# Kernel optimization log

Measured on AMD Instinct MI355X. Metric: run time of the kernel, lower is better.

Reference implementation:

```python
import jax, jax.numpy as jnp
import numpy as np

B, T, N = 16, 1024, 128
WIN, STEP = 30, 2
MOMENT_ORDERS = (2, 4, 8)
D_MODEL = 256


def _mask_diag(corr):
    n = corr.shape[-1]
    eye = jnp.eye(n, dtype=corr.dtype)
    return corr * (1.0 - eye) + eye


def corrcoef_time(xw):
    # xw: [..., L, N] -> corr over channels: [..., N, N]
    L = xw.shape[-2]
    xm = xw - xw.mean(axis=-2, keepdims=True)
    cov = jnp.einsum('...ln,...lm->...nm', xm, xm) / (L - 1 + 1e-8)
    var = jnp.clip(jnp.diagonal(cov, axis1=-2, axis2=-1), 1e-8, None)
    std = jnp.sqrt(var)
    corr = cov / (std[..., :, None] * std[..., None, :])
    corr = jnp.nan_to_num(corr, nan=0.0, posinf=0.0, neginf=0.0)
    return _mask_diag(corr)


def rowwise_corr(M):
    # M: [B, N, F]
    Xc = M - M.mean(axis=-1, keepdims=True)
    num = jnp.einsum('bnf,bmf->bnm', Xc, Xc)
    den1 = jnp.sqrt(jnp.clip((Xc ** 2).sum(axis=-1), 1e-8, None))
    corr = num / (den1[:, :, None] * den1[:, None, :])
    corr = jnp.nan_to_num(corr, nan=0.0, posinf=0.0, neginf=0.0)
    return _mask_diag(corr)


def layer_norm(x, gamma, beta, eps=1e-5):
    mu = x.mean(axis=-1, keepdims=True)
    var = ((x - mu) ** 2).mean(axis=-1, keepdims=True)
    return (x - mu) / jnp.sqrt(var + eps) * gamma + beta


def normalize_adj(adj):
    n = adj.shape[-1]
    A_hat = adj + jnp.eye(n, dtype=adj.dtype)
    d = A_hat.sum(axis=-1)
    dis = jnp.sqrt(1.0 / jnp.clip(d, 1e-8, None))
    return A_hat * dis[:, :, None] * dis[:, None, :]


def setup_inputs() -> dict:
    key = jax.random.key(0)
    ks = jax.random.split(key, 8)
    in_dim = len(MOMENT_ORDERS) * N
    return {
        'x': jax.random.normal(ks[0], (B, T, N), dtype=jnp.float32),
        'ln_gamma': jnp.ones((in_dim,), jnp.float32),
        'ln_beta': jnp.zeros((in_dim,), jnp.float32),
        'W1': jax.random.normal(ks[1], (in_dim, D_MODEL), jnp.float32) * 0.05,
        'b1': jnp.zeros((D_MODEL,), jnp.float32),
        'W2': jax.random.normal(ks[2], (D_MODEL, D_MODEL), jnp.float32) * 0.05,
        'b2': jnp.zeros((D_MODEL,), jnp.float32),
        'Wc': jax.random.normal(ks[3], (D_MODEL, 1), jnp.float32) * 0.05,
        'bc': jnp.zeros((1,), jnp.float32),
    }


def reference(x, ln_gamma, ln_beta, W1, b1, W2, b2, Wc, bc):
    # sliding windows (static indices)
    starts = np.arange(0, T - WIN + 1, STEP)
    idx = starts[:, None] + np.arange(WIN)[None, :]
    xw = x[:, idx, :]
    lo = corrcoef_time(xw)                            # [B, Wn, N, N]

    mean_lo = lo.mean(axis=1, keepdims=True)
    centered = lo - mean_lo
    cm_list, ho_list = [], []
    for d in MOMENT_ORDERS:
        cm = jnp.nan_to_num((centered ** d).mean(axis=1),
                            nan=0.0, posinf=0.0, neginf=0.0)  # [B, N, N]
        cm_list.append(cm)
        ho_list.append(rowwise_corr(cm))

    X = jnp.concatenate(cm_list, axis=-1)             # [B, N, 3N]
    X = layer_norm(X, ln_gamma, ln_beta)

    A = jnp.stack(ho_list, axis=1).mean(axis=1)
    A = 0.5 * (A + jnp.swapaxes(A, 1, 2))
    A_norm = normalize_adj(A)

    H = jax.nn.relu(jnp.einsum('bnm,bmd->bnd', A_norm, X @ W1 + b1))
    H = jax.nn.relu(jnp.einsum('bnm,bmd->bnd', A_norm, H @ W2 + b2))
    g = H.mean(axis=1)                                # [B, d_model]
    out = jax.nn.sigmoid(g @ Wc + bc)                 # [B, 1]
    return out
```

## Files before the change

kernel.cpp:

```cpp
#include <hip/hip_runtime.h>
#include <math.h>

#define BB  16
#define TT  1024
#define NN  128
#define WIN 30
#define NWD 498
#define DM  256
#define IND 384
#define GW  9

#define INV_W (1.0f/498.0f)

#define SARR (BB*NN*NN)

#define OFF_A     0
#define OFF_G     (OFF_A    + BB*NWD*NN)
#define OFF_CM2   (OFF_G    + BB*NWD*NN)
#define OFF_CM4   (OFF_CM2  + SARR)
#define OFF_CM8   (OFF_CM4  + SARR)
#define OFF_PART  (OFF_CM8  + SARR)
#define OFF_ASUM  OFF_PART
#define OFF_ANORM (OFF_ASUM + SARR)
#define OFF_X     (OFF_ANORM + SARR)
#define OFF_BUFA  (OFF_X    + BB*NN*IND)
#define OFF_BUFB  (OFF_BUFA + BB*NN*DM)

__global__ __launch_bounds__(128) void k1_stats(const float* __restrict__ x, float* __restrict__ ws) {
    int bx = blockIdx.x;
    int c = bx & 15, b = bx >> 4;
    int w0 = c*32, w1 = min(NWD, w0+32);
    int n = threadIdx.x;
    const float* xp = x + (size_t)b*TT*NN + n;

    float sum = 0.f, sq = 0.f;
    for (int t = 2*w0; t < 2*w0 + WIN; ++t) {
        float v = xp[(size_t)t*NN];
        sum += v; sq = fmaf(v, v, sq);
    }
    for (int w = w0; w < w1; ++w) {
        if (w > w0) {
            float o0 = xp[(size_t)(2*w-2)*NN], o1 = xp[(size_t)(2*w-1)*NN];
            float n0 = xp[(size_t)(2*w+28)*NN], n1 = xp[(size_t)(2*w+29)*NN];
            sum += (n0 + n1) - (o0 + o1);
            sq  += (n0*n0 + n1*n1) - (o0*o0 + o1*o1);
        }
        float mean = sum * (1.0f/30.0f);
        float ss = sq - 30.0f*mean*mean;
        float var = fmaxf(ss * (1.0f/29.0f), 1e-8f);
        float a = (1.0f / sqrtf(var)) * 0.185695338f;
        ws[OFF_A + ((size_t)b*NWD + w)*NN + n] = a;
        ws[OFF_G + ((size_t)b*NWD + w)*NN + n] = mean * a * 5.477225575f;
    }
}

__global__ __launch_bounds__(256) __attribute__((amdgpu_waves_per_eu(3, 3)))
void k24_inc(const float* __restrict__ x, float* __restrict__ ws) {
    __shared__ __align__(16) float xr[64][NN];
    __shared__ __align__(16) float sa[GW][NN];
    __shared__ __align__(16) float sg[GW][NN];
    int bx = blockIdx.x;
    int wc = bx & 7;
    int slab = (bx >> 3) % 6;
    int b = bx / 48;
    const char IS[6] = {0,0,0,0,1,1};
    const char JS[6] = {0,1,2,3,2,3};
    int is = IS[slab], js = JS[slab];
    int w0 = wc * 63, w1 = min(NWD, w0 + 63);
    int tid = threadIdx.x;
    int jg = tid & 7, ig = tid >> 3;
    int i0 = is*64 + ig*2;
    int j0 = js*32 + jg*4;

    const float* xb = x + (size_t)b*TT*NN;
    const float* Ab = ws + OFF_A + (size_t)b*NWD*NN;
    const float* Gb = ws + OFF_G + (size_t)b*NWD*NN;

    float P[2][4];
    float S1[2][4], S2[2][4], S3[2][4], S4[2][4], S5[2][4], S6[2][4], S7[2][4], S8[2][4];
#pragma unroll
    for (int p=0;p<2;++p)
#pragma unroll
        for (int q=0;q<4;++q) {
            P[p][q]=0.f;
            S1[p][q]=0.f;S2[p][q]=0.f;S3[p][q]=0.f;S4[p][q]=0.f;
            S5[p][q]=0.f;S6[p][q]=0.f;S7[p][q]=0.f;S8[p][q]=0.f;
        }

    auto moments = [&](int k) {
        float2 ai = *(const float2*)&sa[k][i0];
        float2 gi = *(const float2*)&sg[k][i0];
        float4 aj = *(const float4*)&sa[k][j0];
        float4 gj = *(const float4*)&sg[k][j0];
        float av[2] = {ai.x, ai.y};
        float mg[2] = {-gi.x, -gi.y};
        float aw[4] = {aj.x, aj.y, aj.z, aj.w};
        float gw[4] = {gj.x, gj.y, gj.z, gj.w};
#pragma unroll
        for (int p=0;p<2;++p)
#pragma unroll
            for (int q=0;q<4;++q) {
                float aa  = av[p]*aw[q];
                float ngg = mg[p]*gw[q];
                float c   = fmaf(P[p][q], aa, ngg);
                float c2 = c*c;
                float c3 = c2*c;
                float c4 = c2*c2;
                S1[p][q] += c;
                S2[p][q] += c2;
                S3[p][q] += c3;
                S4[p][q] += c4;
                S5[p][q] = fmaf(c4, c,  S5[p][q]);
                S6[p][q] = fmaf(c3, c3, S6[p][q]);
                S7[p][q] = fmaf(c3, c4, S7[p][q]);
                S8[p][q] = fmaf(c4, c4, S8[p][q]);
            }
    };

    int rlo = 2*w0;
    for (int wg = w0; wg < w1; wg += GW) {
        int m = min(GW, w1 - wg);
        __syncthreads();
        int rhi = 2*(wg + m - 1) + 29;
        int nr = rhi - rlo + 1;
        for (int idx = tid; idx < nr*32; idx += 256) {
            int r = idx >> 5, c4 = idx & 31;
            int t = rlo + r;
            *(float4*)&xr[t & 63][c4*4] = ((const float4*)(xb + (size_t)t*NN))[c4];
        }
        for (int idx = tid; idx < m*32; idx += 256) {
            int k = idx >> 5, c4 = idx & 31;
            *(float4*)&sa[k][c4*4] = ((const float4*)(Ab + (size_t)(wg+k)*NN))[c4];
        }
        for (int idx = tid; idx < m*32; idx += 256) {
            int k = idx >> 5, c4 = idx & 31;
            *(float4*)&sg[k][c4*4] = ((const float4*)(Gb + (size_t)(wg+k)*NN))[c4];
        }
        rlo = rhi + 1;
        __syncthreads();

        int kstart = 0;
        if (wg == w0) {
#pragma unroll 6
            for (int k = 0; k < WIN; ++k) {
                int t = 2*w0 + k;
                float2 xi = *(const float2*)&xr[t & 63][i0];
                float4 xj = *(const float4*)&xr[t & 63][j0];
                float av[2] = {xi.x, xi.y};
                float bv[4] = {xj.x, xj.y, xj.z, xj.w};
#pragma unroll
                for (int p=0;p<2;++p)
#pragma unroll
                    for (int q=0;q<4;++q) P[p][q] = fmaf(av[p], bv[q], P[p][q]);
            }
            moments(0);
            kstart = 1;
        }
        for (int k = kstart; k < m; ++k) {
            int w = wg + k;
            int tr[4] = {2*w - 2, 2*w - 1, 2*w + 28, 2*w + 29};
#pragma unroll
            for (int kk = 0; kk < 4; ++kk) {
                int t = tr[kk];
                float sgn = (kk < 2) ? -1.0f : 1.0f;
                float2 xi = *(const float2*)&xr[t & 63][i0];
                float4 xj = *(const float4*)&xr[t & 63][j0];
                float av[2] = {sgn*xi.x, sgn*xi.y};
                float bv[4] = {xj.x, xj.y, xj.z, xj.w};
#pragma unroll
                for (int p=0;p<2;++p)
#pragma unroll
                    for (int q=0;q<4;++q) P[p][q] = fmaf(av[p], bv[q], P[p][q]);
            }
            moments(k);
        }
    }

    float* tp = ws + OFF_PART + (size_t)bx*16384 + tid*8;
#define STORE_ARR(A, S) \
    *(float4*)&tp[(A)*2048]     = make_float4(S[0][0], S[0][1], S[0][2], S[0][3]); \
    *(float4*)&tp[(A)*2048 + 4] = make_float4(S[1][0], S[1][1], S[1][2], S[1][3]);
    STORE_ARR(0, S1) STORE_ARR(1, S2) STORE_ARR(2, S3) STORE_ARR(3, S4)
    STORE_ARR(4, S5) STORE_ARR(5, S6) STORE_ARR(6, S7) STORE_ARR(7, S8)
#undef STORE_ARR
}

__global__ __launch_bounds__(256) void kred(float* __restrict__ ws) {
    int pair = blockIdx.x;
    int b = pair / 6, slab = pair % 6;
    const char IS[6] = {0,0,0,0,1,1};
    const char JS[6] = {0,1,2,3,2,3};
    int is = IS[slab], js = JS[slab];
    int tid = threadIdx.x;
    int jg = tid & 7, ig = tid >> 3;

    float E[8][8];
#pragma unroll
    for (int a=0;a<8;++a)
#pragma unroll
        for (int e=0;e<8;++e) E[a][e] = 0.f;

    for (int c = 0; c < 8; ++c) {
        int bx = (b*6 + slab)*8 + c;
        const float* tp = ws + OFF_PART + (size_t)(b*48 + slab*8 + c)*16384 + tid*8;
        (void)bx;
#pragma unroll
        for (int a=0;a<8;++a) {
            float4 u = *(const float4*)&tp[a*2048];
            float4 v = *(const float4*)&tp[a*2048 + 4];
            E[a][0]+=u.x; E[a][1]+=u.y; E[a][2]+=u.z; E[a][3]+=u.w;
            E[a][4]+=v.x; E[a][5]+=v.y; E[a][6]+=v.z; E[a][7]+=v.w;
        }
    }

    float* C2 = ws + OFF_CM2 + (size_t)b*NN*NN;
    float* C4 = ws + OFF_CM4 + (size_t)b*NN*NN;
    float* C8 = ws + OFF_CM8 + (size_t)b*NN*NN;
#pragma unroll
    for (int p=0;p<2;++p)
#pragma unroll
        for (int q=0;q<4;++q) {
            int e = p*4 + q;
            int i = is*64 + ig*2 + p;
            int j = js*32 + jg*4 + q;
            float cm2, cm4, cm8;
            if (i == j) {
                cm2 = 0.f; cm4 = 0.f; cm8 = 0.f;
            } else {
                float e1 = E[0][e]*INV_W, e2 = E[1][e]*INV_W, e3 = E[2][e]*INV_W, e4 = E[3][e]*INV_W;
                float e5 = E[4][e]*INV_W, e6 = E[5][e]*INV_W, e7 = E[6][e]*INV_W, e8 = E[7][e]*INV_W;
                float m  = e1;
                float m2 = m*m, m3 = m2*m, m4 = m2*m2, m5 = m4*m, m6 = m3*m3, m8 = m4*m4;
                cm2 = e2 - m2;
                cm4 = e4 - 4.f*m*e3 + 6.f*m2*e2 - 3.f*m4;
                cm8 = e8 - 8.f*m*e7 + 28.f*m2*e6 - 56.f*m3*e5 + 70.f*m4*e4
                         - 56.f*m5*e3 + 28.f*m6*e2 - 7.f*m8;
            }
            C2[i*NN + j] = cm2; C2[j*NN + i] = cm2;
            C4[i*NN + j] = cm4; C4[j*NN + i] = cm4;
            C8[i*NN + j] = cm8; C8[j*NN + i] = cm8;
        }
}

__global__ __launch_bounds__(256) void k5_rowcorr(float* __restrict__ ws) {
    __shared__ float Xc[NN][NN+1];
    __shared__ float rmn[NN];
    __shared__ float iden[NN];
    int t = blockIdx.x;
    int jh = t & 1; int di = (t >> 1) % 3; int b = t / 6;
    const float* cm = ws + (di==0 ? OFF_CM2 : (di==1 ? OFF_CM4 : OFF_CM8)) + (size_t)b*NN*NN;
    int tid = threadIdx.x;
    for (int idx = tid; idx < NN*NN; idx += 256) {
        int n = idx >> 7, f = idx & 127;
        Xc[n][f] = cm[idx];
    }
    __syncthreads();
    if (tid < NN) {
        float s = 0.f;
        for (int f = 0; f < NN; ++f) s += Xc[tid][f];
        rmn[tid] = s * (1.0f/NN);
    }
    __syncthreads();
    for (int idx = tid; idx < NN*NN; idx += 256) {
        int n = idx >> 7, f = idx & 127;
        Xc[n][f] -= rmn[n];
    }
    __syncthreads();
    if (tid < NN) {
        float s = 0.f;
        for (int f = 0; f < NN; ++f) { float v = Xc[tid][f]; s = fmaf(v, v, s); }
        iden[tid] = 1.0f/sqrtf(fmaxf(s, 1e-8f));
    }
    __syncthreads();
    int n0 = (tid >> 4)*8, m0 = jh*64 + (tid & 15)*4;
    float acc[8][4];
#pragma unroll
    for (int k=0;k<8;++k)
#pragma unroll
        for (int l=0;l<4;++l) acc[k][l] = 0.f;
    for (int f = 0; f < NN; ++f) {
        float an[8], am[4];
#pragma unroll
        for (int k=0;k<8;++k) an[k] = Xc[n0+k][f];
#pragma unroll
        for (int l=0;l<4;++l) am[l] = Xc[m0+l][f];
#pragma unroll
        for (int k=0;k<8;++k)
#pragma unroll
            for (int l=0;l<4;++l) acc[k][l] = fmaf(an[k], am[l], acc[k][l]);
    }
    float* As = ws + OFF_ASUM + (size_t)b*NN*NN;
#pragma unroll
    for (int k=0;k<8;++k)
#pragma unroll
        for (int l=0;l<4;++l) {
            int gi = n0+k, gj = m0+l;
            float v = acc[k][l]*iden[gi]*iden[gj];
            if (gi == gj) v = 1.0f;
            atomicAdd(&As[gi*NN+gj], v);
        }
}

__global__ __launch_bounds__(256) void k6_anorm(float* __restrict__ ws) {
    __shared__ float As[NN][NN+1];
    __shared__ float dis[NN];
    int b = blockIdx.x;
    const float* Asum = ws + OFF_ASUM + (size_t)b*NN*NN;
    int tid = threadIdx.x;
    for (int idx = tid; idx < NN*NN; idx += 256) {
        int n = idx >> 7, m = idx & 127;
        As[n][m] = (Asum[n*NN+m] + Asum[m*NN+n]) * (1.0f/6.0f);
    }
    __syncthreads();
    if (tid < NN) {
        float d = 1.0f;
        for (int m = 0; m < NN; ++m) d += As[tid][m];
        dis[tid] = sqrtf(1.0f / fmaxf(d, 1e-8f));
    }
    __syncthreads();
    float* An = ws + OFF_ANORM + (size_t)b*NN*NN;
    for (int idx = tid; idx < NN*NN; idx += 256) {
        int n = idx >> 7, m = idx & 127;
        float v = As[n][m] + (n==m ? 1.0f : 0.0f);
        An[idx] = v * dis[n] * dis[m];
    }
}

__global__ __launch_bounds__(128) void k7_ln(const float* __restrict__ gamma, const float* __restrict__ beta,
                                             float* __restrict__ ws) {
    __shared__ float red[128];
    int row = blockIdx.x;
    int tid = threadIdx.x;
    float v0 = ws[OFF_CM2 + (size_t)row*NN + tid];
    float v1 = ws[OFF_CM4 + (size_t)row*NN + tid];
    float v2 = ws[OFF_CM8 + (size_t)row*NN + tid];
    red[tid] = v0+v1+v2;
    __syncthreads();
    for (int o = 64; o > 0; o >>= 1) { if (tid < o) red[tid] += red[tid+o]; __syncthreads(); }
    float mean = red[0] * (1.0f/IND);
    __syncthreads();
    float d0 = v0-mean, d1 = v1-mean, d2 = v2-mean;
    red[tid] = d0*d0 + d1*d1 + d2*d2;
    __syncthreads();
    for (int o = 64; o > 0; o >>= 1) { if (tid < o) red[tid] += red[tid+o]; __syncthreads(); }
    float rstd = 1.0f / sqrtf(red[0]*(1.0f/IND) + 1e-5f);
    float* X = ws + OFF_X + (size_t)row*IND;
    X[tid]     = d0*rstd*gamma[tid]     + beta[tid];
    X[tid+128] = d1*rstd*gamma[tid+128] + beta[tid+128];
    X[tid+256] = d2*rstd*gamma[tid+256] + beta[tid+256];
}

__global__ __launch_bounds__(256) void k8_gemm(const float* __restrict__ Wt, const float* __restrict__ bias,
                                               const float* __restrict__ in, float* __restrict__ out, int K) {
    __shared__ float Xs[8][IND];
    int r0 = blockIdx.x * 8;
    int tid = threadIdx.x;
    for (int r = 0; r < 8; ++r)
        for (int c = tid; c < K; c += 256)
            Xs[r][c] = in[(size_t)(r0+r)*K + c];
    __syncthreads();
    float acc[8];
#pragma unroll
    for (int r = 0; r < 8; ++r) acc[r] = bias[tid];
    for (int k = 0; k < K; ++k) {
        float wv = Wt[(size_t)k*DM + tid];
#pragma unroll
        for (int r = 0; r < 8; ++r) acc[r] = fmaf(Xs[r][k], wv, acc[r]);
    }
#pragma unroll
    for (int r = 0; r < 8; ++r) out[(size_t)(r0+r)*DM + tid] = acc[r];
}

__global__ __launch_bounds__(256) void k9_prop(const float* __restrict__ Anorm, const float* __restrict__ Zin,
                                               float* __restrict__ out) {
    __shared__ float Ar[8][NN];
    int bx = blockIdx.x;
    int b = bx >> 4, n0 = (bx & 15)*8;
    int tid = threadIdx.x;
    const float* A = Anorm + (size_t)b*NN*NN;
    if (tid < NN) {
#pragma unroll
        for (int r = 0; r < 8; ++r) Ar[r][tid] = A[(n0+r)*NN + tid];
    }
    __syncthreads();
    float acc[8] = {0,0,0,0,0,0,0,0};
    const float* Z = Zin + (size_t)b*NN*DM;
    for (int m = 0; m < NN; ++m) {
        float z = Z[(size_t)m*DM + tid];
#pragma unroll
        for (int r = 0; r < 8; ++r) acc[r] = fmaf(Ar[r][m], z, acc[r]);
    }
    float* O = out + (size_t)b*NN*DM;
#pragma unroll
    for (int r = 0; r < 8; ++r) O[(size_t)(n0+r)*DM + tid] = fmaxf(acc[r], 0.0f);
}

__global__ __launch_bounds__(256) void k12_head(const float* __restrict__ H, const float* __restrict__ Wc,
                                                const float* __restrict__ bc, float* __restrict__ outp) {
    __shared__ float red[256];
    int b = blockIdx.x, tid = threadIdx.x;
    float s = 0.f;
    for (int n = 0; n < NN; ++n) s += H[((size_t)b*NN+n)*DM + tid];
    red[tid] = s * (1.0f/NN) * Wc[tid];
    __syncthreads();
    for (int o = 128; o > 0; o >>= 1) { if (tid < o) red[tid] += red[tid+o]; __syncthreads(); }
    if (tid == 0) outp[b] = 1.0f/(1.0f + expf(-(red[0] + bc[0])));
}

extern "C" void kernel_launch(void* const* d_in, const int* in_sizes, int n_in,
                              void* d_out, int out_size, void* d_ws, size_t ws_size,
                              hipStream_t stream) {
    (void)in_sizes; (void)n_in; (void)out_size; (void)ws_size;
    const float* x     = (const float*)d_in[0];
    const float* gamma = (const float*)d_in[1];
    const float* beta  = (const float*)d_in[2];
    const float* W1    = (const float*)d_in[3];
    const float* b1    = (const float*)d_in[4];
    const float* W2    = (const float*)d_in[5];
    const float* b2    = (const float*)d_in[6];
    const float* Wc    = (const float*)d_in[7];
    const float* bc    = (const float*)d_in[8];
    float* ws  = (float*)d_ws;
    float* out = (float*)d_out;

    k1_stats   <<<BB*16,   128, 0, stream>>>(x, ws);
    k24_inc    <<<BB*6*8,  256, 0, stream>>>(x, ws);
    kred       <<<BB*6,    256, 0, stream>>>(ws);
    hipMemsetAsync(ws + OFF_ASUM, 0, (size_t)SARR*sizeof(float), stream);
    k5_rowcorr <<<BB*3*2,  256, 0, stream>>>(ws);
    k6_anorm   <<<BB,      256, 0, stream>>>(ws);
    k7_ln      <<<BB*NN,   128, 0, stream>>>(gamma, beta, ws);
    k8_gemm    <<<BB*NN/8, 256, 0, stream>>>(W1, b1, ws + OFF_X,    ws + OFF_BUFA, IND);
    k9_prop    <<<BB*16,   256, 0, stream>>>(ws + OFF_ANORM, ws + OFF_BUFA, ws + OFF_BUFB);
    k8_gemm    <<<BB*NN/8, 256, 0, stream>>>(W2, b2, ws + OFF_BUFB, ws + OFF_BUFA, DM);
    k9_prop    <<<BB*16,   256, 0, stream>>>(ws + OFF_ANORM, ws + OFF_BUFA, ws + OFF_BUFB);
    k12_head   <<<BB,      256, 0, stream>>>(ws + OFF_BUFB, Wc, bc, out);
}
```

Baseline: 273.5 us.

## Fuse window stats into moment kernel, widen reduction, drop atomics and memset

```diff
diff --git a/kernel.cpp b/kernel.cpp
--- a/kernel.cpp
+++ b/kernel.cpp
@@ -14,51 +14,23 @@
 
 #define SARR (BB*NN*NN)
 
-#define OFF_A     0
-#define OFF_G     (OFF_A    + BB*NWD*NN)
-#define OFF_CM2   (OFF_G    + BB*NWD*NN)
+#define OFF_CM2   0
 #define OFF_CM4   (OFF_CM2  + SARR)
 #define OFF_CM8   (OFF_CM4  + SARR)
-#define OFF_PART  (OFF_CM8  + SARR)
-#define OFF_ASUM  OFF_PART
-#define OFF_ANORM (OFF_ASUM + SARR)
+#define OFF_AD    (OFF_CM8  + SARR)
+#define OFF_PART  (OFF_AD   + 3*SARR)
+#define OFF_ANORM OFF_PART
 #define OFF_X     (OFF_ANORM + SARR)
 #define OFF_BUFA  (OFF_X    + BB*NN*IND)
 #define OFF_BUFB  (OFF_BUFA + BB*NN*DM)
 
-__global__ __launch_bounds__(128) void k1_stats(const float* __restrict__ x, float* __restrict__ ws) {
-    int bx = blockIdx.x;
-    int c = bx & 15, b = bx >> 4;
-    int w0 = c*32, w1 = min(NWD, w0+32);
-    int n = threadIdx.x;
-    const float* xp = x + (size_t)b*TT*NN + n;
-
-    float sum = 0.f, sq = 0.f;
-    for (int t = 2*w0; t < 2*w0 + WIN; ++t) {
-        float v = xp[(size_t)t*NN];
-        sum += v; sq = fmaf(v, v, sq);
-    }
-    for (int w = w0; w < w1; ++w) {
-        if (w > w0) {
-            float o0 = xp[(size_t)(2*w-2)*NN], o1 = xp[(size_t)(2*w-1)*NN];
-            float n0 = xp[(size_t)(2*w+28)*NN], n1 = xp[(size_t)(2*w+29)*NN];
-            sum += (n0 + n1) - (o0 + o1);
-            sq  += (n0*n0 + n1*n1) - (o0*o0 + o1*o1);
-        }
-        float mean = sum * (1.0f/30.0f);
-        float ss = sq - 30.0f*mean*mean;
-        float var = fmaxf(ss * (1.0f/29.0f), 1e-8f);
-        float a = (1.0f / sqrtf(var)) * 0.185695338f;
-        ws[OFF_A + ((size_t)b*NWD + w)*NN + n] = a;
-        ws[OFF_G + ((size_t)b*NWD + w)*NN + n] = mean * a * 5.477225575f;
-    }
-}
-
 __global__ __launch_bounds__(256) __attribute__((amdgpu_waves_per_eu(3, 3)))
 void k24_inc(const float* __restrict__ x, float* __restrict__ ws) {
     __shared__ __align__(16) float xr[64][NN];
-    __shared__ __align__(16) float sa[GW][NN];
-    __shared__ __align__(16) float sg[GW][NN];
+    __shared__ __align__(16) float sa_i[GW][64];
+    __shared__ __align__(16) float sg_i[GW][64];
+    __shared__ __align__(16) float sa_j[GW][32];
+    __shared__ __align__(16) float sg_j[GW][32];
     int bx = blockIdx.x;
     int wc = bx & 7;
     int slab = (bx >> 3) % 6;
@@ -73,8 +45,9 @@
     int j0 = js*32 + jg*4;
 
     const float* xb = x + (size_t)b*TT*NN;
-    const float* Ab = ws + OFF_A + (size_t)b*NWD*NN;
-    const float* Gb = ws + OFF_G + (size_t)b*NWD*NN;
+
+    int ch = (tid < 64) ? (is*64 + tid) : (js*32 + (tid - 64));
+    float rsum = 0.f, rsq = 0.f;
 
     float P[2][4];
     float S1[2][4], S2[2][4], S3[2][4], S4[2][4], S5[2][4], S6[2][4], S7[2][4], S8[2][4];
@@ -87,11 +60,27 @@
             S5[p][q]=0.f;S6[p][q]=0.f;S7[p][q]=0.f;S8[p][q]=0.f;
         }
 
+    auto write_stat = [&](int k) {
+        float mean = rsum * (1.0f/30.0f);
+        float ss = rsq - 30.0f*mean*mean;
+        float var = fmaxf(ss * (1.0f/29.0f), 1e-8f);
+        float a = (1.0f / sqrtf(var)) * 0.185695338f;
+        float g = mean * a * 5.477225575f;
+        if (tid < 64) { sa_i[k][tid] = a; sg_i[k][tid] = g; }
+        else          { sa_j[k][tid-64] = a; sg_j[k][tid-64] = g; }
+    };
+    auto slide = [&](int w) {
+        float o0 = xr[(2*w - 2) & 63][ch], o1 = xr[(2*w - 1) & 63][ch];
+        float n0 = xr[(2*w + 28) & 63][ch], n1 = xr[(2*w + 29) & 63][ch];
+        rsum += (n0 + n1) - (o0 + o1);
+        rsq  += (n0*n0 + n1*n1) - (o0*o0 + o1*o1);
+    };
+
     auto moments = [&](int k) {
-        float2 ai = *(const float2*)&sa[k][i0];
-        float2 gi = *(const float2*)&sg[k][i0];
-        float4 aj = *(const float4*)&sa[k][j0];
-        float4 gj = *(const float4*)&sg[k][j0];
+        float2 ai = *(const float2*)&sa_i[k][ig*2];
+        float2 gi = *(const float2*)&sg_i[k][ig*2];
+        float4 aj = *(const float4*)&sa_j[k][jg*4];
+        float4 gj = *(const float4*)&sg_j[k][jg*4];
         float av[2] = {ai.x, ai.y};
         float mg[2] = {-gi.x, -gi.y};
         float aw[4] = {aj.x, aj.y, aj.z, aj.w};
@@ -128,15 +117,23 @@
             int t = rlo + r;
             *(float4*)&xr[t & 63][c4*4] = ((const float4*)(xb + (size_t)t*NN))[c4];
         }
-        for (int idx = tid; idx < m*32; idx += 256) {
-            int k = idx >> 5, c4 = idx & 31;
-            *(float4*)&sa[k][c4*4] = ((const float4*)(Ab + (size_t)(wg+k)*NN))[c4];
-        }
-        for (int idx = tid; idx < m*32; idx += 256) {
-            int k = idx >> 5, c4 = idx & 31;
-            *(float4*)&sg[k][c4*4] = ((const float4*)(Gb + (size_t)(wg+k)*NN))[c4];
-        }
         rlo = rhi + 1;
+        __syncthreads();
+
+        if (tid < 96) {
+            int kstart = 0;
+            if (wg == w0) {
+                float s = 0.f, q = 0.f;
+                for (int t = 2*w0; t < 2*w0 + WIN; ++t) {
+                    float v = xr[t & 63][ch];
+                    s += v; q = fmaf(v, v, q);
+                }
+                rsum = s; rsq = q;
+                write_stat(0);
+                kstart = 1;
+            }
+            for (int k = kstart; k < m; ++k) { slide(wg + k); write_stat(k); }
+        }
         __syncthreads();
 
         int kstart = 0;
@@ -186,60 +183,48 @@
 }
 
 __global__ __launch_bounds__(256) void kred(float* __restrict__ ws) {
-    int pair = blockIdx.x;
+    int pair = blockIdx.x >> 3, sub = blockIdx.x & 7;
     int b = pair / 6, slab = pair % 6;
     const char IS[6] = {0,0,0,0,1,1};
     const char JS[6] = {0,1,2,3,2,3};
     int is = IS[slab], js = JS[slab];
-    int tid = threadIdx.x;
-    int jg = tid & 7, ig = tid >> 3;
-
-    float E[8][8];
-#pragma unroll
-    for (int a=0;a<8;++a)
-#pragma unroll
-        for (int e=0;e<8;++e) E[a][e] = 0.f;
-
+    int off = sub*256 + threadIdx.x;
+    const float* base = ws + OFF_PART + (size_t)(b*48 + slab*8)*16384;
+
+    float E[8];
+#pragma unroll
+    for (int a=0;a<8;++a) E[a] = 0.f;
     for (int c = 0; c < 8; ++c) {
-        int bx = (b*6 + slab)*8 + c;
-        const float* tp = ws + OFF_PART + (size_t)(b*48 + slab*8 + c)*16384 + tid*8;
-        (void)bx;
-#pragma unroll
-        for (int a=0;a<8;++a) {
-            float4 u = *(const float4*)&tp[a*2048];
-            float4 v = *(const float4*)&tp[a*2048 + 4];
-            E[a][0]+=u.x; E[a][1]+=u.y; E[a][2]+=u.z; E[a][3]+=u.w;
-            E[a][4]+=v.x; E[a][5]+=v.y; E[a][6]+=v.z; E[a][7]+=v.w;
-        }
-    }
-
+        const float* tp = base + (size_t)c*16384;
+#pragma unroll
+        for (int a=0;a<8;++a) E[a] += tp[a*2048 + off];
+    }
+
+    int tid_old = off >> 3, e = off & 7;
+    int ig = tid_old >> 3, jg = tid_old & 7;
+    int p = e >> 2, q = e & 3;
+    int i = is*64 + ig*2 + p;
+    int j = js*32 + jg*4 + q;
+
+    float cm2, cm4, cm8;
+    if (i == j) {
+        cm2 = 0.f; cm4 = 0.f; cm8 = 0.f;
+    } else {
+        float e1 = E[0]*INV_W, e2 = E[1]*INV_W, e3 = E[2]*INV_W, e4 = E[3]*INV_W;
+        float e5 = E[4]*INV_W, e6 = E[5]*INV_W, e7 = E[6]*INV_W, e8 = E[7]*INV_W;
+        float m  = e1;
+        float m2 = m*m, m3 = m2*m, m4 = m2*m2, m5 = m4*m, m6 = m3*m3, m8 = m4*m4;
+        cm2 = e2 - m2;
+        cm4 = e4 - 4.f*m*e3 + 6.f*m2*e2 - 3.f*m4;
+        cm8 = e8 - 8.f*m*e7 + 28.f*m2*e6 - 56.f*m3*e5 + 70.f*m4*e4
+                 - 56.f*m5*e3 + 28.f*m6*e2 - 7.f*m8;
+    }
     float* C2 = ws + OFF_CM2 + (size_t)b*NN*NN;
     float* C4 = ws + OFF_CM4 + (size_t)b*NN*NN;
     float* C8 = ws + OFF_CM8 + (size_t)b*NN*NN;
-#pragma unroll
-    for (int p=0;p<2;++p)
-#pragma unroll
-        for (int q=0;q<4;++q) {
-            int e = p*4 + q;
-            int i = is*64 + ig*2 + p;
-            int j = js*32 + jg*4 + q;
-            float cm2, cm4, cm8;
-            if (i == j) {
-                cm2 = 0.f; cm4 = 0.f; cm8 = 0.f;
-            } else {
-                float e1 = E[0][e]*INV_W, e2 = E[1][e]*INV_W, e3 = E[2][e]*INV_W, e4 = E[3][e]*INV_W;
-                float e5 = E[4][e]*INV_W, e6 = E[5][e]*INV_W, e7 = E[6][e]*INV_W, e8 = E[7][e]*INV_W;
-                float m  = e1;
-                float m2 = m*m, m3 = m2*m, m4 = m2*m2, m5 = m4*m, m6 = m3*m3, m8 = m4*m4;
-                cm2 = e2 - m2;
-                cm4 = e4 - 4.f*m*e3 + 6.f*m2*e2 - 3.f*m4;
-                cm8 = e8 - 8.f*m*e7 + 28.f*m2*e6 - 56.f*m3*e5 + 70.f*m4*e4
-                         - 56.f*m5*e3 + 28.f*m6*e2 - 7.f*m8;
-            }
-            C2[i*NN + j] = cm2; C2[j*NN + i] = cm2;
-            C4[i*NN + j] = cm4; C4[j*NN + i] = cm4;
-            C8[i*NN + j] = cm8; C8[j*NN + i] = cm8;
-        }
+    C2[i*NN + j] = cm2; C2[j*NN + i] = cm2;
+    C4[i*NN + j] = cm4; C4[j*NN + i] = cm4;
+    C8[i*NN + j] = cm8; C8[j*NN + i] = cm8;
 }
 
 __global__ __launch_bounds__(256) void k5_rowcorr(float* __restrict__ ws) {
@@ -289,7 +274,7 @@
 #pragma unroll
             for (int l=0;l<4;++l) acc[k][l] = fmaf(an[k], am[l], acc[k][l]);
     }
-    float* As = ws + OFF_ASUM + (size_t)b*NN*NN;
+    float* Ad = ws + OFF_AD + (size_t)(b*3 + di)*NN*NN;
 #pragma unroll
     for (int k=0;k<8;++k)
 #pragma unroll
@@ -297,7 +282,7 @@
             int gi = n0+k, gj = m0+l;
             float v = acc[k][l]*iden[gi]*iden[gj];
             if (gi == gj) v = 1.0f;
-            atomicAdd(&As[gi*NN+gj], v);
+            Ad[gi*NN + gj] = v;
         }
 }
 
@@ -305,11 +290,15 @@
     __shared__ float As[NN][NN+1];
     __shared__ float dis[NN];
     int b = blockIdx.x;
-    const float* Asum = ws + OFF_ASUM + (size_t)b*NN*NN;
+    const float* A0 = ws + OFF_AD + (size_t)(b*3 + 0)*NN*NN;
+    const float* A1 = ws + OFF_AD + (size_t)(b*3 + 1)*NN*NN;
+    const float* A2 = ws + OFF_AD + (size_t)(b*3 + 2)*NN*NN;
     int tid = threadIdx.x;
     for (int idx = tid; idx < NN*NN; idx += 256) {
         int n = idx >> 7, m = idx & 127;
-        As[n][m] = (Asum[n*NN+m] + Asum[m*NN+n]) * (1.0f/6.0f);
+        int ji = m*NN + n;
+        float s = A0[idx] + A0[ji] + A1[idx] + A1[ji] + A2[idx] + A2[ji];
+        As[n][m] = s * (1.0f/6.0f);
     }
     __syncthreads();
     if (tid < NN) {
@@ -362,6 +351,7 @@
     float acc[8];
 #pragma unroll
     for (int r = 0; r < 8; ++r) acc[r] = bias[tid];
+#pragma unroll 4
     for (int k = 0; k < K; ++k) {
         float wv = Wt[(size_t)k*DM + tid];
 #pragma unroll
@@ -385,6 +375,7 @@
     __syncthreads();
     float acc[8] = {0,0,0,0,0,0,0,0};
     const float* Z = Zin + (size_t)b*NN*DM;
+#pragma unroll 4
     for (int m = 0; m < NN; ++m) {
         float z = Z[(size_t)m*DM + tid];
 #pragma unroll
@@ -423,10 +414,8 @@
     float* ws  = (float*)d_ws;
     float* out = (float*)d_out;
 
-    k1_stats   <<<BB*16,   128, 0, stream>>>(x, ws);
     k24_inc    <<<BB*6*8,  256, 0, stream>>>(x, ws);
-    kred       <<<BB*6,    256, 0, stream>>>(ws);
-    hipMemsetAsync(ws + OFF_ASUM, 0, (size_t)SARR*sizeof(float), stream);
+    kred       <<<BB*6*8,  256, 0, stream>>>(ws);
     k5_rowcorr <<<BB*3*2,  256, 0, stream>>>(ws);
     k6_anorm   <<<BB,      256, 0, stream>>>(ws);
     k7_ln      <<<BB*NN,   128, 0, stream>>>(gamma, beta, ws);
```

Result: slower. 279.1 us (+2.0%).

## Fuse layernorm with first GEMM, prop with second GEMM; drop atomics and memset

Applied to the files above, without the earlier changes.

```diff
diff --git a/kernel.cpp b/kernel.cpp
--- a/kernel.cpp
+++ b/kernel.cpp
@@ -19,11 +19,10 @@
 #define OFF_CM2   (OFF_G    + BB*NWD*NN)
 #define OFF_CM4   (OFF_CM2  + SARR)
 #define OFF_CM8   (OFF_CM4  + SARR)
-#define OFF_PART  (OFF_CM8  + SARR)
-#define OFF_ASUM  OFF_PART
-#define OFF_ANORM (OFF_ASUM + SARR)
-#define OFF_X     (OFF_ANORM + SARR)
-#define OFF_BUFA  (OFF_X    + BB*NN*IND)
+#define OFF_AD    (OFF_CM8  + SARR)
+#define OFF_PART  (OFF_AD   + 3*SARR)
+#define OFF_ANORM OFF_PART
+#define OFF_BUFA  (OFF_ANORM + SARR)
 #define OFF_BUFB  (OFF_BUFA + BB*NN*DM)
 
 __global__ __launch_bounds__(128) void k1_stats(const float* __restrict__ x, float* __restrict__ ws) {
@@ -186,60 +185,48 @@
 }
 
 __global__ __launch_bounds__(256) void kred(float* __restrict__ ws) {
-    int pair = blockIdx.x;
+    int pair = blockIdx.x >> 3, sub = blockIdx.x & 7;
     int b = pair / 6, slab = pair % 6;
     const char IS[6] = {0,0,0,0,1,1};
     const char JS[6] = {0,1,2,3,2,3};
     int is = IS[slab], js = JS[slab];
-    int tid = threadIdx.x;
-    int jg = tid & 7, ig = tid >> 3;
-
-    float E[8][8];
-#pragma unroll
-    for (int a=0;a<8;++a)
-#pragma unroll
-        for (int e=0;e<8;++e) E[a][e] = 0.f;
-
+    int off = sub*256 + threadIdx.x;
+    const float* base = ws + OFF_PART + (size_t)(b*48 + slab*8)*16384;
+
+    float E[8];
+#pragma unroll
+    for (int a=0;a<8;++a) E[a] = 0.f;
     for (int c = 0; c < 8; ++c) {
-        int bx = (b*6 + slab)*8 + c;
-        const float* tp = ws + OFF_PART + (size_t)(b*48 + slab*8 + c)*16384 + tid*8;
-        (void)bx;
-#pragma unroll
-        for (int a=0;a<8;++a) {
-            float4 u = *(const float4*)&tp[a*2048];
-            float4 v = *(const float4*)&tp[a*2048 + 4];
-            E[a][0]+=u.x; E[a][1]+=u.y; E[a][2]+=u.z; E[a][3]+=u.w;
-            E[a][4]+=v.x; E[a][5]+=v.y; E[a][6]+=v.z; E[a][7]+=v.w;
-        }
-    }
-
+        const float* tp = base + (size_t)c*16384;
+#pragma unroll
+        for (int a=0;a<8;++a) E[a] += tp[a*2048 + off];
+    }
+
+    int tid_old = off >> 3, e = off & 7;
+    int ig = tid_old >> 3, jg = tid_old & 7;
+    int p = e >> 2, q = e & 3;
+    int i = is*64 + ig*2 + p;
+    int j = js*32 + jg*4 + q;
+
+    float cm2, cm4, cm8;
+    if (i == j) {
+        cm2 = 0.f; cm4 = 0.f; cm8 = 0.f;
+    } else {
+        float e1 = E[0]*INV_W, e2 = E[1]*INV_W, e3 = E[2]*INV_W, e4 = E[3]*INV_W;
+        float e5 = E[4]*INV_W, e6 = E[5]*INV_W, e7 = E[6]*INV_W, e8 = E[7]*INV_W;
+        float m  = e1;
+        float m2 = m*m, m3 = m2*m, m4 = m2*m2, m5 = m4*m, m6 = m3*m3, m8 = m4*m4;
+        cm2 = e2 - m2;
+        cm4 = e4 - 4.f*m*e3 + 6.f*m2*e2 - 3.f*m4;
+        cm8 = e8 - 8.f*m*e7 + 28.f*m2*e6 - 56.f*m3*e5 + 70.f*m4*e4
+                 - 56.f*m5*e3 + 28.f*m6*e2 - 7.f*m8;
+    }
     float* C2 = ws + OFF_CM2 + (size_t)b*NN*NN;
     float* C4 = ws + OFF_CM4 + (size_t)b*NN*NN;
     float* C8 = ws + OFF_CM8 + (size_t)b*NN*NN;
-#pragma unroll
-    for (int p=0;p<2;++p)
-#pragma unroll
-        for (int q=0;q<4;++q) {
-            int e = p*4 + q;
-            int i = is*64 + ig*2 + p;
-            int j = js*32 + jg*4 + q;
-            float cm2, cm4, cm8;
-            if (i == j) {
-                cm2 = 0.f; cm4 = 0.f; cm8 = 0.f;
-            } else {
-                float e1 = E[0][e]*INV_W, e2 = E[1][e]*INV_W, e3 = E[2][e]*INV_W, e4 = E[3][e]*INV_W;
-                float e5 = E[4][e]*INV_W, e6 = E[5][e]*INV_W, e7 = E[6][e]*INV_W, e8 = E[7][e]*INV_W;
-                float m  = e1;
-                float m2 = m*m, m3 = m2*m, m4 = m2*m2, m5 = m4*m, m6 = m3*m3, m8 = m4*m4;
-                cm2 = e2 - m2;
-                cm4 = e4 - 4.f*m*e3 + 6.f*m2*e2 - 3.f*m4;
-                cm8 = e8 - 8.f*m*e7 + 28.f*m2*e6 - 56.f*m3*e5 + 70.f*m4*e4
-                         - 56.f*m5*e3 + 28.f*m6*e2 - 7.f*m8;
-            }
-            C2[i*NN + j] = cm2; C2[j*NN + i] = cm2;
-            C4[i*NN + j] = cm4; C4[j*NN + i] = cm4;
-            C8[i*NN + j] = cm8; C8[j*NN + i] = cm8;
-        }
+    C2[i*NN + j] = cm2; C2[j*NN + i] = cm2;
+    C4[i*NN + j] = cm4; C4[j*NN + i] = cm4;
+    C8[i*NN + j] = cm8; C8[j*NN + i] = cm8;
 }
 
 __global__ __launch_bounds__(256) void k5_rowcorr(float* __restrict__ ws) {
@@ -289,7 +276,7 @@
 #pragma unroll
             for (int l=0;l<4;++l) acc[k][l] = fmaf(an[k], am[l], acc[k][l]);
     }
-    float* As = ws + OFF_ASUM + (size_t)b*NN*NN;
+    float* Ad = ws + OFF_AD + (size_t)(b*3 + di)*NN*NN;
 #pragma unroll
     for (int k=0;k<8;++k)
 #pragma unroll
@@ -297,7 +284,7 @@
             int gi = n0+k, gj = m0+l;
             float v = acc[k][l]*iden[gi]*iden[gj];
             if (gi == gj) v = 1.0f;
-            atomicAdd(&As[gi*NN+gj], v);
+            Ad[gi*NN + gj] = v;
         }
 }
 
@@ -305,11 +292,15 @@
     __shared__ float As[NN][NN+1];
     __shared__ float dis[NN];
     int b = blockIdx.x;
-    const float* Asum = ws + OFF_ASUM + (size_t)b*NN*NN;
+    const float* A0 = ws + OFF_AD + (size_t)(b*3 + 0)*NN*NN;
+    const float* A1 = ws + OFF_AD + (size_t)(b*3 + 1)*NN*NN;
+    const float* A2 = ws + OFF_AD + (size_t)(b*3 + 2)*NN*NN;
     int tid = threadIdx.x;
     for (int idx = tid; idx < NN*NN; idx += 256) {
         int n = idx >> 7, m = idx & 127;
-        As[n][m] = (Asum[n*NN+m] + Asum[m*NN+n]) * (1.0f/6.0f);
+        int ji = m*NN + n;
+        float s = A0[idx] + A0[ji] + A1[idx] + A1[ji] + A2[idx] + A2[ji];
+        As[n][m] = s * (1.0f/6.0f);
     }
     __syncthreads();
     if (tid < NN) {
@@ -326,81 +317,131 @@
     }
 }
 
-__global__ __launch_bounds__(128) void k7_ln(const float* __restrict__ gamma, const float* __restrict__ beta,
-                                             float* __restrict__ ws) {
-    __shared__ float red[128];
-    int row = blockIdx.x;
-    int tid = threadIdx.x;
-    float v0 = ws[OFF_CM2 + (size_t)row*NN + tid];
-    float v1 = ws[OFF_CM4 + (size_t)row*NN + tid];
-    float v2 = ws[OFF_CM8 + (size_t)row*NN + tid];
-    red[tid] = v0+v1+v2;
-    __syncthreads();
-    for (int o = 64; o > 0; o >>= 1) { if (tid < o) red[tid] += red[tid+o]; __syncthreads(); }
-    float mean = red[0] * (1.0f/IND);
-    __syncthreads();
-    float d0 = v0-mean, d1 = v1-mean, d2 = v2-mean;
-    red[tid] = d0*d0 + d1*d1 + d2*d2;
-    __syncthreads();
-    for (int o = 64; o > 0; o >>= 1) { if (tid < o) red[tid] += red[tid+o]; __syncthreads(); }
-    float rstd = 1.0f / sqrtf(red[0]*(1.0f/IND) + 1e-5f);
-    float* X = ws + OFF_X + (size_t)row*IND;
-    X[tid]     = d0*rstd*gamma[tid]     + beta[tid];
-    X[tid+128] = d1*rstd*gamma[tid+128] + beta[tid+128];
-    X[tid+256] = d2*rstd*gamma[tid+256] + beta[tid+256];
-}
-
-__global__ __launch_bounds__(256) void k8_gemm(const float* __restrict__ Wt, const float* __restrict__ bias,
-                                               const float* __restrict__ in, float* __restrict__ out, int K) {
+__global__ __launch_bounds__(256) void k78_lngemm(const float* __restrict__ gamma, const float* __restrict__ beta,
+                                                  const float* __restrict__ W1, const float* __restrict__ b1,
+                                                  float* __restrict__ ws) {
     __shared__ float Xs[8][IND];
+    __shared__ float smean[8], srstd[8];
     int r0 = blockIdx.x * 8;
     int tid = threadIdx.x;
-    for (int r = 0; r < 8; ++r)
-        for (int c = tid; c < K; c += 256)
-            Xs[r][c] = in[(size_t)(r0+r)*K + c];
+    for (int r = 0; r < 8; ++r) {
+        int row = r0 + r;
+        int b = row >> 7, n = row & 127;
+        const float* c2 = ws + OFF_CM2 + ((size_t)b*NN + n)*NN;
+        const float* c4 = ws + OFF_CM4 + ((size_t)b*NN + n)*NN;
+        const float* c8 = ws + OFF_CM8 + ((size_t)b*NN + n)*NN;
+        for (int c = tid; c < IND; c += 256)
+            Xs[r][c] = (c < 128) ? c2[c] : (c < 256) ? c4[c-128] : c8[c-256];
+    }
+    __syncthreads();
+    {
+        int team = tid >> 5, lane = tid & 31;
+        float s = 0.f;
+        for (int c = lane; c < IND; c += 32) s += Xs[team][c];
+#pragma unroll
+        for (int o = 16; o > 0; o >>= 1) s += __shfl_down(s, o, 32);
+        float mean = __shfl(s, 0, 32) * (1.0f/IND);
+        float v = 0.f;
+        for (int c = lane; c < IND; c += 32) { float d = Xs[team][c] - mean; v = fmaf(d, d, v); }
+#pragma unroll
+        for (int o = 16; o > 0; o >>= 1) v += __shfl_down(v, o, 32);
+        if (lane == 0) {
+            smean[team] = mean;
+            srstd[team] = 1.0f / sqrtf(v*(1.0f/IND) + 1e-5f);
+        }
+    }
+    __syncthreads();
+    for (int r = 0; r < 8; ++r) {
+        float mean = smean[r], rstd = srstd[r];
+        for (int c = tid; c < IND; c += 256)
+            Xs[r][c] = (Xs[r][c] - mean)*rstd*gamma[c] + beta[c];
+    }
     __syncthreads();
     float acc[8];
-#pragma unroll
-    for (int r = 0; r < 8; ++r) acc[r] = bias[tid];
-    for (int k = 0; k < K; ++k) {
-        float wv = Wt[(size_t)k*DM + tid];
+    float bv = b1[tid];
+#pragma unroll
+    for (int r = 0; r < 8; ++r) acc[r] = bv;
+#pragma unroll 4
+    for (int k = 0; k < IND; ++k) {
+        float wv = W1[(size_t)k*DM + tid];
 #pragma unroll
         for (int r = 0; r < 8; ++r) acc[r] = fmaf(Xs[r][k], wv, acc[r]);
     }
-#pragma unroll
-    for (int r = 0; r < 8; ++r) out[(size_t)(r0+r)*DM + tid] = acc[r];
-}
-
-__global__ __launch_bounds__(256) void k9_prop(const float* __restrict__ Anorm, const float* __restrict__ Zin,
-                                               float* __restrict__ out) {
+    float* O = ws + OFF_BUFA;
+#pragma unroll
+    for (int r = 0; r < 8; ++r) O[(size_t)(r0+r)*DM + tid] = acc[r];
+}
+
+__global__ __launch_bounds__(256) void k98_propgemm(const float* __restrict__ W2, const float* __restrict__ b2,
+                                                    float* __restrict__ ws) {
+    __shared__ float Ar[8][NN];
+    __shared__ float Hs[8][DM];
+    int bx = blockIdx.x;
+    int b = bx >> 4, n0 = (bx & 15)*8;
+    int tid = threadIdx.x;
+    const float* A = ws + OFF_ANORM + (size_t)b*NN*NN;
+    if (tid < NN) {
+#pragma unroll
+        for (int r = 0; r < 8; ++r) Ar[r][tid] = A[(n0+r)*NN + tid];
+    }
+    __syncthreads();
+    float acc[8] = {0,0,0,0,0,0,0,0};
+    const float* Z = ws + OFF_BUFA + (size_t)b*NN*DM;
+#pragma unroll 4
+    for (int m = 0; m < NN; ++m) {
+        float z = Z[(size_t)m*DM + tid];
+#pragma unroll
+        for (int r = 0; r < 8; ++r) acc[r] = fmaf(Ar[r][m], z, acc[r]);
+    }
+#pragma unroll
+    for (int r = 0; r < 8; ++r) Hs[r][tid] = fmaxf(acc[r], 0.0f);
+    __syncthreads();
+    float acc2[8];
+    float bv = b2[tid];
+#pragma unroll
+    for (int r = 0; r < 8; ++r) acc2[r] = bv;
+#pragma unroll 4
+    for (int k = 0; k < DM; ++k) {
+        float wv = W2[(size_t)k*DM + tid];
+#pragma unroll
+        for (int r = 0; r < 8; ++r) acc2[r] = fmaf(Hs[r][k], wv, acc2[r]);
+    }
+    float* O = ws + OFF_BUFB + (size_t)b*NN*DM;
+#pragma unroll
+    for (int r = 0; r < 8; ++r) O[(size_t)(n0+r)*DM + tid] = acc2[r];
+}
+
+__global__ __launch_bounds__(256) void k9_prop(float* __restrict__ ws) {
     __shared__ float Ar[8][NN];
     int bx = blockIdx.x;
     int b = bx >> 4, n0 = (bx & 15)*8;
     int tid = threadIdx.x;
-    const float* A = Anorm + (size_t)b*NN*NN;
+    const float* A = ws + OFF_ANORM + (size_t)b*NN*NN;
     if (tid < NN) {
 #pragma unroll
         for (int r = 0; r < 8; ++r) Ar[r][tid] = A[(n0+r)*NN + tid];
     }
     __syncthreads();
     float acc[8] = {0,0,0,0,0,0,0,0};
-    const float* Z = Zin + (size_t)b*NN*DM;
+    const float* Z = ws + OFF_BUFB + (size_t)b*NN*DM;
+#pragma unroll 4
     for (int m = 0; m < NN; ++m) {
         float z = Z[(size_t)m*DM + tid];
 #pragma unroll
         for (int r = 0; r < 8; ++r) acc[r] = fmaf(Ar[r][m], z, acc[r]);
     }
-    float* O = out + (size_t)b*NN*DM;
+    float* O = ws + OFF_BUFA + (size_t)b*NN*DM;
 #pragma unroll
     for (int r = 0; r < 8; ++r) O[(size_t)(n0+r)*DM + tid] = fmaxf(acc[r], 0.0f);
 }
 
-__global__ __launch_bounds__(256) void k12_head(const float* __restrict__ H, const float* __restrict__ Wc,
-                                                const float* __restrict__ bc, float* __restrict__ outp) {
+__global__ __launch_bounds__(256) void k12_head(const float* __restrict__ Wc, const float* __restrict__ bc,
+                                                float* __restrict__ ws, float* __restrict__ outp) {
     __shared__ float red[256];
     int b = blockIdx.x, tid = threadIdx.x;
+    const float* H = ws + OFF_BUFA + (size_t)b*NN*DM;
     float s = 0.f;
-    for (int n = 0; n < NN; ++n) s += H[((size_t)b*NN+n)*DM + tid];
+    for (int n = 0; n < NN; ++n) s += H[(size_t)n*DM + tid];
     red[tid] = s * (1.0f/NN) * Wc[tid];
     __syncthreads();
     for (int o = 128; o > 0; o >>= 1) { if (tid < o) red[tid] += red[tid+o]; __syncthreads(); }
@@ -425,14 +466,11 @@
 
     k1_stats   <<<BB*16,   128, 0, stream>>>(x, ws);
     k24_inc    <<<BB*6*8,  256, 0, stream>>>(x, ws);
-    kred       <<<BB*6,    256, 0, stream>>>(ws);
-    hipMemsetAsync(ws + OFF_ASUM, 0, (size_t)SARR*sizeof(float), stream);
+    kred       <<<BB*6*8,  256, 0, stream>>>(ws);
     k5_rowcorr <<<BB*3*2,  256, 0, stream>>>(ws);
     k6_anorm   <<<BB,      256, 0, stream>>>(ws);
-    k7_ln      <<<BB*NN,   128, 0, stream>>>(gamma, beta, ws);
-    k8_gemm    <<<BB*NN/8, 256, 0, stream>>>(W1, b1, ws + OFF_X,    ws + OFF_BUFA, IND);
-    k9_prop    <<<BB*16,   256, 0, stream>>>(ws + OFF_ANORM, ws + OFF_BUFA, ws + OFF_BUFB);
-    k8_gemm    <<<BB*NN/8, 256, 0, stream>>>(W2, b2, ws + OFF_BUFB, ws + OFF_BUFA, DM);
-    k9_prop    <<<BB*16,   256, 0, stream>>>(ws + OFF_ANORM, ws + OFF_BUFA, ws + OFF_BUFB);
-    k12_head   <<<BB,      256, 0, stream>>>(ws + OFF_BUFB, Wc, bc, out);
-}
+    k78_lngemm <<<BB*NN/8, 256, 0, stream>>>(gamma, beta, W1, b1, ws);
+    k98_propgemm<<<BB*16,  256, 0, stream>>>(W2, b2, ws);
+    k9_prop    <<<BB*16,   256, 0, stream>>>(ws);
+    k12_head   <<<BB,      256, 0, stream>>>(Wc, bc, ws, out);
+}
```

Result: no change. 278.8 us (+1.9%).
